# Optimization experiments

Hardware: AMD Instinct MI355X
Metric: run time of the kernel (lower is better)

The kernel has to match this reference:

```python
import jax, jax.numpy as jnp
import numpy as np

EPS = 1e-5

def _ln(x, g, b):
    m = x.mean(-1, keepdims=True)
    v = jnp.var(x, axis=-1, keepdims=True)
    return (x - m) / jnp.sqrt(v + EPS) * g + b

def _forward(x, W_Q, W_K, W_V, W_O, ffn1_w, ffn1_b, ffn2_w, ffn2_b,
             ln1_g, ln1_b, ln2_g, ln2_b):
    B, C, H, W = x.shape
    nh, _, hd = W_Q.shape
    xl = x.transpose(0, 2, 3, 1)                      # [B,H,W,C]
    # per-head projections: [B,H,W,nh,hd]
    Q = jnp.einsum('bijc,hcd->bijhd', xl, W_Q)
    K = jnp.einsum('bijc,hcd->bijhd', xl, W_K)
    V = jnp.einsum('bijc,hcd->bijhd', xl, W_V)
    Hi, Wi = H - 2, W - 2
    Qc = Q[:, 1:H - 1, 1:W - 1]                       # interior queries
    # stack the 9 shifted views = 3x3 neighborhoods, row-major (i*3+j order)
    Kw = jnp.stack([K[:, di:di + Hi, dj:dj + Wi]
                    for di in range(3) for dj in range(3)], axis=3)  # [B,Hi,Wi,9,nh,hd]
    Vw = jnp.stack([V[:, di:di + Hi, dj:dj + Wi]
                    for di in range(3) for dj in range(3)], axis=3)
    scale = jnp.asarray(hd, x.dtype) ** 0.5
    attn = jnp.einsum('bijhd,bijnhd->bijnh', Qc, Kw) / scale
    attn = jax.nn.softmax(attn, axis=3)               # softmax over the 9 neighbors
    out = jnp.einsum('bijnh,bijnhd->bijhd', attn, Vw).reshape(B, Hi, Wi, nh * hd)
    out = out @ W_O                                   # output projection, [B,Hi,Wi,C]
    y = jnp.pad(out, ((0, 0), (1, 1), (1, 1), (0, 0)))  # border pixels stay zero
    y = jax.nn.relu(_ln(y, ln1_g, ln1_b))
    y = jax.nn.relu(y @ ffn1_w.T + ffn1_b)            # [B,H,W,9C]
    y = y @ ffn2_w.T + ffn2_b                         # [B,H,W,C]
    y = _ln(y, ln2_g, ln2_b)
    y = jax.nn.relu(y + xl)                           # identity shortcut (stride=1, C_in==C_out)
    return y.transpose(0, 3, 1, 2)                    # back to NCHW


def setup_inputs() -> dict:
    key = jax.random.key(0)
    ks = jax.random.split(key, 8)
    B, C, H, W, nh, hd = 8, 288, 48, 48, 9, 32
    Cff = C * 9
    f32 = jnp.float32
    return {
        'x': jax.random.normal(ks[0], (B, C, H, W), f32),
        'W_Q': jax.random.uniform(ks[1], (nh, C, hd), f32, -0.1, 0.1),
        'W_K': jax.random.uniform(ks[2], (nh, C, hd), f32, -0.1, 0.1),
        'W_V': jax.random.normal(ks[3], (nh, C, hd), f32) * 0.05,
        'W_O': jnp.eye(C, dtype=f32),
        'ffn1_w': jax.random.normal(ks[4], (Cff, C), f32) * 0.02,
        'ffn1_b': jnp.zeros((Cff,), f32),
        'ffn2_w': jax.random.normal(ks[5], (C, Cff), f32) * 0.02,
        'ffn2_b': jnp.zeros((C,), f32),
        'ln1_g': jnp.ones((C,), f32),
        'ln1_b': jnp.zeros((C,), f32),
        'ln2_g': jnp.ones((C,), f32),
        'ln2_b': jnp.zeros((C,), f32),
    }


def reference(x, W_Q, W_K, W_V, W_O, ffn1_w, ffn1_b, ffn2_w, ffn2_b,
              ln1_g, ln1_b, ln2_g, ln2_b):
    return _forward(x, W_Q, W_K, W_V, W_O, ffn1_w, ffn1_b, ffn2_w, ffn2_b,
                    ln1_g, ln1_b, ln2_g, ln2_b)
```

## Files before the change

### kernel.cpp

```cpp
#include <hip/hip_runtime.h>
#include <hip/hip_bf16.h>

static constexpr int Bn = 8, Cc = 288, Hh = 48, Ww = 48;
static constexpr int HW = Hh * Ww;
static constexpr int Mtot = Bn * HW;
static constexpr int NH = 9, HD = 32;
static constexpr int Cff = 2592;
static constexpr int CffP = 2688;
static constexpr int NQKV = 896;

typedef __attribute__((ext_vector_type(8))) short bf16x8;
typedef __attribute__((ext_vector_type(4))) float f32x4;
typedef __attribute__((ext_vector_type(4))) unsigned short u16x4;

typedef const __attribute__((address_space(1))) unsigned gmem_word;
typedef __attribute__((address_space(3))) unsigned lds_word;

__device__ __forceinline__ void gload16(const void* g, void* l) {
    __builtin_amdgcn_global_load_lds((gmem_word*)g, (lds_word*)l, 16, 0, 0);
}

__device__ __forceinline__ int swz(int byte) {
    return byte ^ (((byte >> 7) & 7) << 4);
}

__device__ __forceinline__ float bf2f(unsigned short u) {
    return __bfloat162float(*(__hip_bfloat16*)&u);
}

__global__ __launch_bounds__(256) void transpose_in(const float* __restrict__ x,
                                                    __hip_bfloat16* __restrict__ xlb) {
    __shared__ float tile[32][33];
    int b = blockIdx.z;
    int c0 = blockIdx.y * 32;
    int p0 = blockIdx.x * 32;
    int tx = threadIdx.x, ty = threadIdx.y;
#pragma unroll
    for (int q = 0; q < 4; ++q) {
        int c = c0 + ty + q * 8;
        tile[ty + q * 8][tx] = x[((size_t)b * Cc + c) * HW + p0 + tx];
    }
    __syncthreads();
#pragma unroll
    for (int q = 0; q < 4; ++q) {
        int p = p0 + ty + q * 8;
        xlb[((size_t)b * HW + p) * Cc + c0 + tx] = __float2bfloat16(tile[tx][ty + q * 8]);
    }
}

__global__ __launch_bounds__(256) void repack_qkvt(const float* __restrict__ WQ,
                                                   const float* __restrict__ WK,
                                                   const float* __restrict__ WV,
                                                   __hip_bfloat16* __restrict__ Wt) {
    int t = blockIdx.x * 256 + threadIdx.x;
    if (t >= NQKV * Cc) return;
    int n = t / Cc;
    int c = t % Cc;
    if (n >= 3 * Cc) { Wt[t] = __float2bfloat16(0.f); return; }
    int g = n / Cc;
    int r = n % Cc;
    int h = r / HD, d = r % HD;
    const float* W = (g == 0) ? WQ : ((g == 1) ? WK : WV);
    Wt[t] = __float2bfloat16(W[((size_t)h * Cc + c) * HD + d]);
}

__global__ __launch_bounds__(256) void repack_wot(const float* __restrict__ WO,
                                                  __hip_bfloat16* __restrict__ Wt) {
    int t = blockIdx.x * 256 + threadIdx.x;
    if (t >= Cc * Cc) return;
    int n = t / Cc;
    int c = t % Cc;
    Wt[t] = __float2bfloat16(WO[(size_t)c * Cc + n]);
}

__global__ __launch_bounds__(256) void pad_w1(const float* __restrict__ w, __hip_bfloat16* __restrict__ o) {
    int t = blockIdx.x * 256 + threadIdx.x;
    if (t >= CffP * Cc) return;
    o[t] = __float2bfloat16(t < Cff * Cc ? w[t] : 0.f);
}

__global__ __launch_bounds__(256) void pad_w2(const float* __restrict__ w, __hip_bfloat16* __restrict__ o) {
    int t = blockIdx.x * 256 + threadIdx.x;
    if (t >= Cc * CffP) return;
    int n = t / CffP, c = t % CffP;
    o[t] = __float2bfloat16(c < Cff ? w[(size_t)n * Cff + c] : 0.f);
}

__global__ __launch_bounds__(256) void pad_b1(const float* __restrict__ b, float* __restrict__ o) {
    int t = blockIdx.x * 256 + threadIdx.x;
    if (t < CffP) o[t] = (t < Cff) ? b[t] : 0.f;
}

template <int BM, int BN, bool OUT_BF16, bool BIAS, bool RELU>
__global__ __launch_bounds__(256) void gemm_mfma(const __hip_bfloat16* __restrict__ A,
                                                 const __hip_bfloat16* __restrict__ Bw,
                                                 const float* __restrict__ bias,
                                                 void* __restrict__ Cout,
                                                 int M, int N, int K, int ldk) {
    constexpr int MR = BM / 32;
    constexpr int NF = BN / 32;
    constexpr int CA = BM / 16;
    constexpr int CB = BN / 16;
    __shared__ __hip_bfloat16 As[2][BM * 32];
    __shared__ __hip_bfloat16 Bs[2][BN * 32];
    const int gx = gridDim.x, gy = gridDim.y;
    const int nwg = gx * gy * gridDim.z;
    int lin = blockIdx.x + gx * (blockIdx.y + gy * blockIdx.z);
    lin = (lin & 7) * (nwg >> 3) + (lin >> 3);
    const int bz = lin / (gx * gy);
    const int rem = lin - bz * gx * gy;
    const int by = rem / gx;
    const int bx = rem - by * gx;

    const int tid = threadIdx.x;
    const int wave = tid >> 6, lane = tid & 63;
    const int l16 = lane & 15, lq = lane >> 4;
    const int wr = wave >> 1, wc = wave & 1;
    const int bm = by * BM;
    const int bn = bx * BN;
    const int nt = K >> 5;
    const size_t kz2 = (size_t)bz * K * 2;
    const char* Ab = (const char*)A + kz2;
    const char* Bb = (const char*)Bw + kz2;
    const size_t ldk2 = (size_t)ldk * 2;

    f32x4 acc[MR][NF] = {};

    auto stage = [&](int buf, int t) {
        const size_t k0b = (size_t)(t << 5) * 2;
        for (int c = wave; c < CA + CB; c += 4) {
            if (c < CA) {
                int s = (c << 10) + lane * 16;
                int u = swz(s);
                int row = u >> 6, koff = u & 63;
                gload16(Ab + (size_t)(bm + row) * ldk2 + k0b + koff, &As[buf][c << 9]);
            } else {
                int s = ((c - CA) << 10) + lane * 16;
                int u = swz(s);
                int row = u >> 6, koff = u & 63;
                gload16(Bb + (size_t)(bn + row) * ldk2 + k0b + koff, &Bs[buf][(c - CA) << 9]);
            }
        }
    };

    int aoff[MR], boff[NF];
#pragma unroll
    for (int m = 0; m < MR; ++m)
        aoff[m] = swz((wr * (BM / 2) + m * 16 + l16) * 64 + lq * 16);
#pragma unroll
    for (int n = 0; n < NF; ++n)
        boff[n] = swz((wc * (BN / 2) + n * 16 + l16) * 64 + lq * 16);

    stage(0, 0);
    __syncthreads();
    int cur = 0;
    for (int t = 0; t < nt; ++t) {
        if (t + 1 < nt) stage(cur ^ 1, t + 1);
        const char* Ac = (const char*)&As[cur][0];
        const char* Bc = (const char*)&Bs[cur][0];
        bf16x8 a[MR], b[NF];
#pragma unroll
        for (int m = 0; m < MR; ++m) a[m] = *(const bf16x8*)(Ac + aoff[m]);
#pragma unroll
        for (int n = 0; n < NF; ++n) b[n] = *(const bf16x8*)(Bc + boff[n]);
#pragma unroll
        for (int m = 0; m < MR; ++m)
#pragma unroll
            for (int n = 0; n < NF; ++n)
                acc[m][n] = __builtin_amdgcn_mfma_f32_16x16x32_bf16(a[m], b[n], acc[m][n], 0, 0, 0);
        __syncthreads();
        cur ^= 1;
    }

    const size_t plane = (size_t)bz * M * N;
#pragma unroll
    for (int m = 0; m < MR; ++m) {
#pragma unroll
        for (int n = 0; n < NF; ++n) {
            const int col = bn + wc * (BN / 2) + n * 16 + l16;
            const float bv = BIAS ? bias[col] : 0.f;
#pragma unroll
            for (int r = 0; r < 4; ++r) {
                const int row = bm + wr * (BM / 2) + m * 16 + lq * 4 + r;
                float v = acc[m][n][r] + bv;
                if (RELU) v = fmaxf(v, 0.f);
                if (OUT_BF16)
                    ((__hip_bfloat16*)Cout)[plane + (size_t)row * N + col] = __float2bfloat16(v);
                else
                    ((float*)Cout)[plane + (size_t)row * N + col] = v;
            }
        }
    }
}

template <bool BIAS>
__global__ __launch_bounds__(256) void gemm_ln(const __hip_bfloat16* __restrict__ A,
                                               const __hip_bfloat16* __restrict__ Bw,
                                               const float* __restrict__ bias,
                                               const float* __restrict__ gam,
                                               const float* __restrict__ bet,
                                               __hip_bfloat16* __restrict__ dst,
                                               int K) {
    __shared__ __hip_bfloat16 As[2][32 * 32];
    __shared__ __hip_bfloat16 Bs[2][288 * 32];
    __shared__ float red[2][2][32];
    const int tid = threadIdx.x;
    const int wave = tid >> 6, lane = tid & 63;
    const int l16 = lane & 15, lq = lane >> 4;
    const int wr = wave >> 1, wc = wave & 1;
    const int bm = blockIdx.x * 32;
    const int nt = K >> 5;
    const char* Ab = (const char*)A;
    const char* Bb = (const char*)Bw;
    const size_t Ks2 = (size_t)K * 2;

    f32x4 acc[9] = {};

    auto stage = [&](int buf, int t) {
        const size_t k0b = (size_t)(t << 5) * 2;
        for (int c = wave; c < 20; c += 4) {
            if (c < 2) {
                int s = (c << 10) + lane * 16;
                int u = swz(s);
                int row = u >> 6, koff = u & 63;
                gload16(Ab + (size_t)(bm + row) * Ks2 + k0b + koff, &As[buf][c << 9]);
            } else {
                int s = ((c - 2) << 10) + lane * 16;
                int u = swz(s);
                int row = u >> 6, koff = u & 63;
                gload16(Bb + (size_t)row * Ks2 + k0b + koff, &Bs[buf][(c - 2) << 9]);
            }
        }
    };

    const int aoff = swz((wr * 16 + l16) * 64 + lq * 16);
    int boff[9];
#pragma unroll
    for (int n = 0; n < 9; ++n)
        boff[n] = swz((wc * 144 + n * 16 + l16) * 64 + lq * 16);

    stage(0, 0);
    __syncthreads();
    int cur = 0;
    for (int t = 0; t < nt; ++t) {
        if (t + 1 < nt) stage(cur ^ 1, t + 1);
        const char* Ac = (const char*)&As[cur][0];
        const char* Bc = (const char*)&Bs[cur][0];
        bf16x8 a = *(const bf16x8*)(Ac + aoff);
        bf16x8 b[9];
#pragma unroll
        for (int n = 0; n < 9; ++n) b[n] = *(const bf16x8*)(Bc + boff[n]);
#pragma unroll
        for (int n = 0; n < 9; ++n)
            acc[n] = __builtin_amdgcn_mfma_f32_16x16x32_bf16(a, b[n], acc[n], 0, 0, 0);
        __syncthreads();
        cur ^= 1;
    }

    if (BIAS) {
#pragma unroll
        for (int n = 0; n < 9; ++n) {
            const float bv = bias[wc * 144 + n * 16 + l16];
#pragma unroll
            for (int r = 0; r < 4; ++r) acc[n][r] += bv;
        }
    }
    float sum[4] = {0.f, 0.f, 0.f, 0.f}, sq[4] = {0.f, 0.f, 0.f, 0.f};
#pragma unroll
    for (int n = 0; n < 9; ++n)
#pragma unroll
        for (int r = 0; r < 4; ++r) { sum[r] += acc[n][r]; sq[r] += acc[n][r] * acc[n][r]; }
#pragma unroll
    for (int s = 8; s >= 1; s >>= 1) {
#pragma unroll
        for (int r = 0; r < 4; ++r) { sum[r] += __shfl_xor(sum[r], s); sq[r] += __shfl_xor(sq[r], s); }
    }
    if (l16 == 0) {
#pragma unroll
        for (int r = 0; r < 4; ++r) {
            red[0][wc][wr * 16 + lq * 4 + r] = sum[r];
            red[1][wc][wr * 16 + lq * 4 + r] = sq[r];
        }
    }
    __syncthreads();
    float mean[4], rstd[4];
#pragma unroll
    for (int r = 0; r < 4; ++r) {
        const int rl = wr * 16 + lq * 4 + r;
        const float S = red[0][0][rl] + red[0][1][rl];
        const float Q = red[1][0][rl] + red[1][1][rl];
        mean[r] = S * (1.f / Cc);
        rstd[r] = rsqrtf(Q * (1.f / Cc) - mean[r] * mean[r] + 1e-5f);
    }
#pragma unroll
    for (int n = 0; n < 9; ++n) {
        const int col = wc * 144 + n * 16 + l16;
        const float gm = gam[col], bt = bet[col];
#pragma unroll
        for (int r = 0; r < 4; ++r) {
            const int row = bm + wr * 16 + lq * 4 + r;
            float y = (acc[n][r] - mean[r]) * rstd[r] * gm + bt;
            dst[(size_t)row * Cc + col] = __float2bfloat16(fmaxf(y, 0.f));
        }
    }
}

__global__ __launch_bounds__(256) void attn_kernel(const __hip_bfloat16* __restrict__ qkv,
                                                   __hip_bfloat16* __restrict__ aout) {
    int t = blockIdx.x * 256 + threadIdx.x;
    int d = t & 31;
    int ph = t >> 5;
    if (ph >= 16928 * 9) return;
    int h = ph % 9;
    int pix = ph / 9;
    int b = pix / (46 * 46);
    int r = pix % (46 * 46);
    int i = r / 46 + 1;
    int j = r % 46 + 1;
    int m = b * HW + i * Ww + j;
    int hd = h * HD + d;
    float q = __bfloat162float(qkv[(size_t)m * NQKV + hd]);
    float logits[9];
    int mns[9];
#pragma unroll
    for (int n = 0; n < 9; ++n) {
        int di = n / 3, dj = n % 3;
        int mn = b * HW + (i - 1 + di) * Ww + (j - 1 + dj);
        mns[n] = mn;
        float kv = __bfloat162float(qkv[(size_t)mn * NQKV + 288 + hd]);
        float p = q * kv;
#pragma unroll
        for (int s = 16; s >= 1; s >>= 1) p += __shfl_xor(p, s);
        logits[n] = p * 0.17677669529663687f;
    }
    float mx = logits[0];
#pragma unroll
    for (int n = 1; n < 9; ++n) mx = fmaxf(mx, logits[n]);
    float w[9];
    float sum = 0.f;
#pragma unroll
    for (int n = 0; n < 9; ++n) { w[n] = expf(logits[n] - mx); sum += w[n]; }
    float inv = 1.f / sum;
    float o = 0.f;
#pragma unroll
    for (int n = 0; n < 9; ++n)
        o += w[n] * __bfloat162float(qkv[(size_t)mns[n] * NQKV + 576 + hd]);
    aout[(size_t)m * Cc + hd] = __float2bfloat16(o * inv);
}

__global__ __launch_bounds__(256) void final_kernel(const __hip_bfloat16* __restrict__ part,
                                                    const float* __restrict__ fb2,
                                                    const __hip_bfloat16* __restrict__ xlb,
                                                    const float* __restrict__ g,
                                                    const float* __restrict__ bta,
                                                    float* __restrict__ out) {
    __shared__ float T[32][289];
    const int tid = threadIdx.x;
    const int wave = tid >> 6, lane = tid & 63;
    const int p0 = blockIdx.x * 32;
    const int b = p0 / HW;
    const int p = p0 % HW;
    const size_t plane = (size_t)Mtot * Cc;
    const unsigned short* pt = (const unsigned short*)part;
    const unsigned short* xr = (const unsigned short*)xlb;

    for (int it = 0; it < 8; ++it) {
        const int pw = wave * 8 + it;
        const size_t base = (size_t)(p0 + pw) * Cc;
        const int c0 = lane * 4;
        const int c1 = 256 + lane * 4;
        float v0[4], v1[4];
        {
            u16x4 a = *(const u16x4*)(pt + base + c0);
            u16x4 bb = *(const u16x4*)(pt + plane + base + c0);
            u16x4 cc = *(const u16x4*)(pt + 2 * plane + base + c0);
#pragma unroll
            for (int j = 0; j < 4; ++j)
                v0[j] = bf2f(a[j]) + bf2f(bb[j]) + bf2f(cc[j]) + fb2[c0 + j];
        }
        if (lane < 8) {
            u16x4 a = *(const u16x4*)(pt + base + c1);
            u16x4 bb = *(const u16x4*)(pt + plane + base + c1);
            u16x4 cc = *(const u16x4*)(pt + 2 * plane + base + c1);
#pragma unroll
            for (int j = 0; j < 4; ++j)
                v1[j] = bf2f(a[j]) + bf2f(bb[j]) + bf2f(cc[j]) + fb2[c1 + j];
        } else {
#pragma unroll
            for (int j = 0; j < 4; ++j) v1[j] = 0.f;
        }
        float sum = 0.f, sq = 0.f;
#pragma unroll
        for (int j = 0; j < 4; ++j) {
            sum += v0[j] + v1[j];
            sq += v0[j] * v0[j] + v1[j] * v1[j];
        }
#pragma unroll
        for (int s = 32; s >= 1; s >>= 1) { sum += __shfl_xor(sum, s); sq += __shfl_xor(sq, s); }
        const float mean = sum * (1.f / Cc);
        const float rstd = rsqrtf(sq * (1.f / Cc) - mean * mean + 1e-5f);
        {
            u16x4 xv = *(const u16x4*)(xr + base + c0);
#pragma unroll
            for (int j = 0; j < 4; ++j) {
                float y = (v0[j] - mean) * rstd * g[c0 + j] + bta[c0 + j];
                T[pw][c0 + j] = fmaxf(y + bf2f(xv[j]), 0.f);
            }
        }
        if (lane < 8) {
            u16x4 xv = *(const u16x4*)(xr + base + c1);
#pragma unroll
            for (int j = 0; j < 4; ++j) {
                float y = (v1[j] - mean) * rstd * g[c1 + j] + bta[c1 + j];
                T[pw][c1 + j] = fmaxf(y + bf2f(xv[j]), 0.f);
            }
        }
    }
    __syncthreads();
#pragma unroll
    for (int k = 0; k < 36; ++k) {
        const int idx = k * 256 + tid;
        const int c = idx >> 5, pw = idx & 31;
        out[((size_t)b * Cc + c) * HW + p + pw] = T[pw][c];
    }
}

__global__ void sentinel_kernel(float* out, float val) {
    out[threadIdx.x] = val;
}

extern "C" void kernel_launch(void* const* d_in, const int* in_sizes, int n_in,
                              void* d_out, int out_size, void* d_ws, size_t ws_size,
                              hipStream_t stream) {
    const float* x   = (const float*)d_in[0];
    const float* WQ  = (const float*)d_in[1];
    const float* WK  = (const float*)d_in[2];
    const float* WV  = (const float*)d_in[3];
    const float* WO  = (const float*)d_in[4];
    const float* f1w = (const float*)d_in[5];
    const float* f1b = (const float*)d_in[6];
    const float* f2w = (const float*)d_in[7];
    const float* f2b = (const float*)d_in[8];
    const float* g1  = (const float*)d_in[9];
    const float* b1  = (const float*)d_in[10];
    const float* g2  = (const float*)d_in[11];
    const float* b2  = (const float*)d_in[12];

    char* ws = (char*)d_ws;
    size_t off = 0;
    auto alloc = [&](size_t bytes) { void* p = ws + off; off += (bytes + 255) & ~(size_t)255; return p; };

    __hip_bfloat16* xlb   = (__hip_bfloat16*)alloc((size_t)Mtot * Cc * 2);
    __hip_bfloat16* wqkvt = (__hip_bfloat16*)alloc((size_t)NQKV * Cc * 2);
    __hip_bfloat16* qkv   = (__hip_bfloat16*)alloc((size_t)Mtot * NQKV * 2);
    __hip_bfloat16* aout  = (__hip_bfloat16*)alloc((size_t)Mtot * Cc * 2);
    __hip_bfloat16* wot   = (__hip_bfloat16*)alloc((size_t)Cc * Cc * 2);
    __hip_bfloat16* yln   = (__hip_bfloat16*)alloc((size_t)Mtot * Cc * 2);
    __hip_bfloat16* w1b   = (__hip_bfloat16*)alloc((size_t)CffP * Cc * 2);
    float*          b1p   = (float*)alloc((size_t)CffP * 4);
    __hip_bfloat16* mid   = (__hip_bfloat16*)alloc((size_t)Mtot * CffP * 2);
    __hip_bfloat16* w2b   = (__hip_bfloat16*)alloc((size_t)Cc * CffP * 2);
    __hip_bfloat16* f2o3  = (__hip_bfloat16*)alloc((size_t)3 * Mtot * Cc * 2);

    if (ws_size < off) {
        sentinel_kernel<<<1, 256, 0, stream>>>((float*)d_out, (float)off * 1e-6f);
        return;
    }

    transpose_in<<<dim3(HW / 32, Cc / 32, Bn), dim3(32, 8), 0, stream>>>(x, xlb);
    repack_qkvt<<<(NQKV * Cc + 255) / 256, 256, 0, stream>>>(WQ, WK, WV, wqkvt);
    repack_wot<<<(Cc * Cc + 255) / 256, 256, 0, stream>>>(WO, wot);
    pad_w1<<<(CffP * Cc + 255) / 256, 256, 0, stream>>>(f1w, w1b);
    pad_w2<<<(Cc * CffP + 255) / 256, 256, 0, stream>>>(f2w, w2b);
    pad_b1<<<(CffP + 255) / 256, 256, 0, stream>>>(f1b, b1p);

    gemm_mfma<128, 128, true, false, false><<<dim3(NQKV / 128, Mtot / 128, 1), 256, 0, stream>>>(
        xlb, wqkvt, nullptr, qkv, Mtot, NQKV, Cc, Cc);

    hipMemsetAsync(aout, 0, (size_t)Mtot * Cc * 2, stream);
    attn_kernel<<<(16928 * 9 * 32) / 256, 256, 0, stream>>>(qkv, aout);

    gemm_ln<false><<<Mtot / 32, 256, 0, stream>>>(
        aout, wot, nullptr, g1, b1, yln, Cc);

    gemm_mfma<128, 128, true, true, true><<<dim3(CffP / 128, Mtot / 128, 1), 256, 0, stream>>>(
        yln, w1b, b1p, mid, Mtot, CffP, Cc, Cc);

    gemm_mfma<128, 96, true, false, false><<<dim3(Cc / 96, Mtot / 128, 3), 256, 0, stream>>>(
        mid, w2b, nullptr, f2o3, Mtot, Cc, CffP / 3, CffP);

    final_kernel<<<Mtot / 32, 256, 0, stream>>>(f2o3, f2b, xlb, g2, b2, (float*)d_out);
}
```

Baseline: 220.8 us.

## Prefetch two K-tiles ahead with explicit vmcnt waits in MFMA GEMMs

Both GEMM kernels now issue loads for tiles t and t+1 before the loop. Each iteration waits with a partial s_waitcnt vmcnt so only the current tile's global-to-LDS loads must finish, and the next tile's loads stay in flight. This replaces __syncthreads with raw s_barrier and refills the just-consumed buffer two tiles ahead, aiming to hide global-load latency better than the previous one-ahead double buffer. MFMA sections are also wrapped in s_setprio to favour math-issuing waves. The risk is correctness: the hand-computed vmcnt counts must match each wave's actual number of outstanding loads.

```diff
diff --git a/kernel.cpp b/kernel.cpp
--- a/kernel.cpp
+++ b/kernel.cpp
@@ -18,6 +18,11 @@
 
 __device__ __forceinline__ void gload16(const void* g, void* l) {
     __builtin_amdgcn_global_load_lds((gmem_word*)g, (lds_word*)l, 16, 0, 0);
+}
+
+template <int N>
+__device__ __forceinline__ void vmwait() {
+    asm volatile("s_waitcnt vmcnt(%0)" :: "n"(N) : "memory");
 }
 
 __device__ __forceinline__ int swz(int byte) {
@@ -101,6 +106,7 @@
     constexpr int NF = BN / 32;
     constexpr int CA = BM / 16;
     constexpr int CB = BN / 16;
+    constexpr int TOT = CA + CB;
     __shared__ __hip_bfloat16 As[2][BM * 32];
     __shared__ __hip_bfloat16 Bs[2][BN * 32];
     const int gx = gridDim.x, gy = gridDim.y;
@@ -128,7 +134,7 @@
 
     auto stage = [&](int buf, int t) {
         const size_t k0b = (size_t)(t << 5) * 2;
-        for (int c = wave; c < CA + CB; c += 4) {
+        for (int c = wave; c < TOT; c += 4) {
             if (c < CA) {
                 int s = (c << 10) + lane * 16;
                 int u = swz(s);
@@ -152,10 +158,18 @@
         boff[n] = swz((wc * (BN / 2) + n * 16 + l16) * 64 + lq * 16);
 
     stage(0, 0);
-    __syncthreads();
+    stage(1, 1);
     int cur = 0;
     for (int t = 0; t < nt; ++t) {
-        if (t + 1 < nt) stage(cur ^ 1, t + 1);
+        if (t == nt - 1) {
+            vmwait<0>();
+        } else if constexpr ((TOT & 3) == 0) {
+            vmwait<TOT / 4>();
+        } else {
+            if (wave < (TOT & 3)) vmwait<(TOT + 3) / 4>();
+            else                  vmwait<TOT / 4>();
+        }
+        __builtin_amdgcn_s_barrier();
         const char* Ac = (const char*)&As[cur][0];
         const char* Bc = (const char*)&Bs[cur][0];
         bf16x8 a[MR], b[NF];
@@ -163,12 +177,15 @@
         for (int m = 0; m < MR; ++m) a[m] = *(const bf16x8*)(Ac + aoff[m]);
 #pragma unroll
         for (int n = 0; n < NF; ++n) b[n] = *(const bf16x8*)(Bc + boff[n]);
+        __builtin_amdgcn_s_setprio(1);
 #pragma unroll
         for (int m = 0; m < MR; ++m)
 #pragma unroll
             for (int n = 0; n < NF; ++n)
                 acc[m][n] = __builtin_amdgcn_mfma_f32_16x16x32_bf16(a[m], b[n], acc[m][n], 0, 0, 0);
-        __syncthreads();
+        __builtin_amdgcn_s_setprio(0);
+        __builtin_amdgcn_s_barrier();
+        if (t + 2 < nt) stage(cur, t + 2);
         cur ^= 1;
     }
 
@@ -240,20 +257,25 @@
         boff[n] = swz((wc * 144 + n * 16 + l16) * 64 + lq * 16);
 
     stage(0, 0);
-    __syncthreads();
+    stage(1, 1);
     int cur = 0;
     for (int t = 0; t < nt; ++t) {
-        if (t + 1 < nt) stage(cur ^ 1, t + 1);
+        if (t == nt - 1) vmwait<0>();
+        else             vmwait<5>();
+        __builtin_amdgcn_s_barrier();
         const char* Ac = (const char*)&As[cur][0];
         const char* Bc = (const char*)&Bs[cur][0];
         bf16x8 a = *(const bf16x8*)(Ac + aoff);
         bf16x8 b[9];
 #pragma unroll
         for (int n = 0; n < 9; ++n) b[n] = *(const bf16x8*)(Bc + boff[n]);
+        __builtin_amdgcn_s_setprio(1);
 #pragma unroll
         for (int n = 0; n < 9; ++n)
             acc[n] = __builtin_amdgcn_mfma_f32_16x16x32_bf16(a, b[n], acc[n], 0, 0, 0);
-        __syncthreads();
+        __builtin_amdgcn_s_setprio(0);
+        __builtin_amdgcn_s_barrier();
+        if (t + 2 < nt) stage(cur, t + 2);
         cur ^= 1;
     }
 
```

Measured after the change: 217.0 us. About the same (-1.7%).
